# Kernel optimization log

Measured on AMD Instinct MI355X. Metric: run time of the kernel, lower is better.

The kernel has to match this reference:

```python
import jax, jax.numpy as jnp
import numpy as np

N = 100000
E = 1600000
F_IN = 16
HEADS = 4
OUT_CH = 32  # conv_filters[i] // heads = 128 // 4
HID = HEADS * OUT_CH  # 128
N_GRAPHS = 64
N_TARGETS = 4
EPS_BN = 1e-5


def setup_inputs() -> dict:
    key = jax.random.key(0)
    ks = jax.random.split(key, 32)
    glorot = lambda k, shp: jax.random.normal(k, shp, jnp.float32) * np.sqrt(2.0 / (shp[0] + shp[-1]))
    inp = {
        "node_features": jax.random.normal(ks[0], (N, F_IN), jnp.float32),
        "edge_index": jax.random.randint(ks[1], (2, E), 0, N, jnp.int64),
        "batch": jnp.sort(jax.random.randint(ks[2], (N,), 0, N_GRAPHS, jnp.int64)),
        # GAT layer 1: F_IN -> HEADS*OUT_CH
        "W1": glorot(ks[3], (F_IN, HID)),
        "b1": jnp.zeros((HID,), jnp.float32),
        "att_src1": glorot(ks[4], (HEADS, OUT_CH)),
        "att_dst1": glorot(ks[5], (HEADS, OUT_CH)),
        "bn_g1": jnp.ones((HID,), jnp.float32),
        "bn_b1": jnp.zeros((HID,), jnp.float32),
        # GAT layer 2: HID -> HID
        "W2": glorot(ks[6], (HID, HID)),
        "b2": jnp.zeros((HID,), jnp.float32),
        "att_src2": glorot(ks[7], (HEADS, OUT_CH)),
        "att_dst2": glorot(ks[8], (HEADS, OUT_CH)),
        "bn_g2": jnp.ones((HID,), jnp.float32),
        "bn_b2": jnp.zeros((HID,), jnp.float32),
        # dense head 128 -> 64 -> 32 -> 4
        "d1_W": glorot(ks[9], (HID, HID // 2)),
        "d1_b": jnp.zeros((HID // 2,), jnp.float32),
        "bn_g_d1": jnp.ones((HID // 2,), jnp.float32),
        "bn_b_d1": jnp.zeros((HID // 2,), jnp.float32),
        "d2_W": glorot(ks[10], (HID // 2, HID // 4)),
        "d2_b": jnp.zeros((HID // 4,), jnp.float32),
        "bn_g_d2": jnp.ones((HID // 4,), jnp.float32),
        "bn_b_d2": jnp.zeros((HID // 4,), jnp.float32),
        "fc_W": glorot(ks[11], (HID // 4, N_TARGETS)),
        "fc_b": jnp.zeros((N_TARGETS,), jnp.float32),
    }
    return inp


def batch_norm(x, gamma, beta):
    # training-mode BatchNorm1d: biased batch stats over dim 0
    mu = jnp.mean(x, axis=0)
    var = jnp.mean(jnp.square(x - mu), axis=0)
    return gamma * (x - mu) * jax.lax.rsqrt(var + EPS_BN) + beta


def gat_conv(x, src, dst, W, b, att_src, att_dst):
    # PyG GATConv (shared lin, concat heads): h = x @ W -> [N, H, C]
    h = (x @ W).reshape(-1, HEADS, OUT_CH)
    a_s = jnp.sum(h * att_src, axis=-1)  # [N, H]
    a_d = jnp.sum(h * att_dst, axis=-1)  # [N, H]
    e = jax.nn.leaky_relu(a_s[src] + a_d[dst], 0.2)  # [E, H]
    # softmax over incoming edges per destination node
    m = jax.ops.segment_max(e, dst, num_segments=N)
    m = jnp.where(jnp.isfinite(m), m, 0.0)
    w = jnp.exp(e - m[dst])
    s = jax.ops.segment_sum(w, dst, num_segments=N)
    alpha = w / (s[dst] + 1e-16)  # [E, H]
    out = jax.ops.segment_sum(h[src] * alpha[:, :, None], dst, num_segments=N)
    return out.reshape(-1, HID) + b


def reference(node_features, edge_index, batch,
              W1, b1, att_src1, att_dst1, bn_g1, bn_b1,
              W2, b2, att_src2, att_dst2, bn_g2, bn_b2,
              d1_W, d1_b, bn_g_d1, bn_b_d1,
              d2_W, d2_b, bn_g_d2, bn_b_d2,
              fc_W, fc_b):
    src, dst = edge_index[0], edge_index[1]
    x = gat_conv(node_features, src, dst, W1, b1, att_src1, att_dst1)
    x = jax.nn.relu(batch_norm(x, bn_g1, bn_b1))
    x = gat_conv(x, src, dst, W2, b2, att_src2, att_dst2)
    x = jax.nn.relu(batch_norm(x, bn_g2, bn_b2))
    # global mean pool over graphs
    sums = jax.ops.segment_sum(x, batch, num_segments=N_GRAPHS)
    cnt = jax.ops.segment_sum(jnp.ones((x.shape[0],), x.dtype), batch, num_segments=N_GRAPHS)
    g = sums / jnp.maximum(cnt, 1.0)[:, None]  # [G, HID]
    g = jax.nn.relu(batch_norm(g @ d1_W + d1_b, bn_g_d1, bn_b_d1))
    g = jax.nn.relu(batch_norm(g @ d2_W + d2_b, bn_g_d2, bn_b_d2))
    return g @ fc_W + fc_b
```

## Files before the change

### kernel.cpp

```cpp
#include <hip/hip_runtime.h>

#define HID 128
#define NG 64

__device__ __forceinline__ float lrelu(float v) { return v > 0.0f ? v : 0.2f * v; }

__device__ __forceinline__ unsigned int bf16rne(float f) {
    unsigned int u = __float_as_uint(f);
    return (u + 0x7fffu + ((u >> 16) & 1u)) >> 16;
}
__device__ __forceinline__ unsigned int packbf(float a, float b) {
    return bf16rne(a) | (bf16rne(b) << 16);
}

template <int K, bool BN>
__global__ __launch_bounds__(256) void k_gemm(const float* __restrict__ xin,
        const float* __restrict__ W,
        const double* __restrict__ bnsum, const float* __restrict__ gamma, const float* __restrict__ beta,
        const float* __restrict__ attS, const float* __restrict__ attD,
        unsigned short* __restrict__ h, float* __restrict__ as_, float* __restrict__ ad_, int N)
{
    __shared__ float xs[64][K];
    __shared__ __align__(16) float sc_s[K];
    __shared__ __align__(16) float sh_s[K];
    constexpr int K4 = K / 4;
    int t = threadIdx.x;
    int cq = t & 31;
    int nr = t >> 5;

    if (BN) {
        if (t < K) {
            double mu = bnsum[t] / (double)N;
            double var = bnsum[K + t] / (double)N - mu * mu;
            if (var < 0.0) var = 0.0;
            double rs = 1.0 / sqrt(var + 1e-5);
            float sc = (float)((double)gamma[t] * rs);
            sc_s[t] = sc;
            sh_s[t] = beta[t] - (float)mu * sc;
        }
        __syncthreads();
    }

    float4 atS = ((const float4*)attS)[cq];
    float4 atD = ((const float4*)attD)[cq];

    for (int n0 = blockIdx.x * 64; n0 < N; n0 += gridDim.x * 64) {
        int nrem = N - n0; if (nrem > 64) nrem = 64;
        for (int idx = t; idx < 64 * K4; idx += 256) {
            int n = idx / K4, k4 = idx % K4;
            float4 v = make_float4(0.f, 0.f, 0.f, 0.f);
            if (n < nrem) {
                v = ((const float4*)(xin + (size_t)(n0 + n) * K))[k4];
                if (BN) {
                    float4 sc = ((const float4*)sc_s)[k4];
                    float4 sh = ((const float4*)sh_s)[k4];
                    v.x = fmaf(v.x, sc.x, sh.x); v.x = v.x > 0.f ? v.x : 0.f;
                    v.y = fmaf(v.y, sc.y, sh.y); v.y = v.y > 0.f ? v.y : 0.f;
                    v.z = fmaf(v.z, sc.z, sh.z); v.z = v.z > 0.f ? v.z : 0.f;
                    v.w = fmaf(v.w, sc.w, sh.w); v.w = v.w > 0.f ? v.w : 0.f;
                }
            }
            *(float4*)(&xs[n][k4 * 4]) = v;
        }
        __syncthreads();

        float4 acc[8];
#pragma unroll
        for (int j = 0; j < 8; ++j) acc[j] = make_float4(0.f, 0.f, 0.f, 0.f);

        const float4* W4 = (const float4*)W;
#pragma unroll 2
        for (int k4 = 0; k4 < K4; ++k4) {
            float4 w0 = W4[(k4 * 4 + 0) * 32 + cq];
            float4 w1 = W4[(k4 * 4 + 1) * 32 + cq];
            float4 w2 = W4[(k4 * 4 + 2) * 32 + cq];
            float4 w3 = W4[(k4 * 4 + 3) * 32 + cq];
#pragma unroll
            for (int j = 0; j < 8; ++j) {
                float4 xv = *(const float4*)(&xs[nr * 8 + j][k4 * 4]);
                acc[j].x = fmaf(xv.x, w0.x, acc[j].x);
                acc[j].y = fmaf(xv.x, w0.y, acc[j].y);
                acc[j].z = fmaf(xv.x, w0.z, acc[j].z);
                acc[j].w = fmaf(xv.x, w0.w, acc[j].w);
                acc[j].x = fmaf(xv.y, w1.x, acc[j].x);
                acc[j].y = fmaf(xv.y, w1.y, acc[j].y);
                acc[j].z = fmaf(xv.y, w1.z, acc[j].z);
                acc[j].w = fmaf(xv.y, w1.w, acc[j].w);
                acc[j].x = fmaf(xv.z, w2.x, acc[j].x);
                acc[j].y = fmaf(xv.z, w2.y, acc[j].y);
                acc[j].z = fmaf(xv.z, w2.z, acc[j].z);
                acc[j].w = fmaf(xv.z, w2.w, acc[j].w);
                acc[j].x = fmaf(xv.w, w3.x, acc[j].x);
                acc[j].y = fmaf(xv.w, w3.y, acc[j].y);
                acc[j].z = fmaf(xv.w, w3.z, acc[j].z);
                acc[j].w = fmaf(xv.w, w3.w, acc[j].w);
            }
        }

#pragma unroll
        for (int j = 0; j < 8; ++j) {
            int n = nr * 8 + j;
            bool ok = (n < nrem);
            if (ok) {
                unsigned int lo = packbf(acc[j].x, acc[j].y);
                unsigned int hi = packbf(acc[j].z, acc[j].w);
                ((uint2*)(h + (size_t)(n0 + n) * 128))[cq] = make_uint2(lo, hi);
            }
            float ps = acc[j].x * atS.x + acc[j].y * atS.y + acc[j].z * atS.z + acc[j].w * atS.w;
            float pd = acc[j].x * atD.x + acc[j].y * atD.y + acc[j].z * atD.z + acc[j].w * atD.w;
            ps += __shfl_xor(ps, 1); pd += __shfl_xor(pd, 1);
            ps += __shfl_xor(ps, 2); pd += __shfl_xor(pd, 2);
            ps += __shfl_xor(ps, 4); pd += __shfl_xor(pd, 4);
            if (ok && (cq & 7) == 0) {
                int hd = cq >> 3;
                as_[(size_t)(n0 + n) * 4 + hd] = ps;
                ad_[(size_t)(n0 + n) * 4 + hd] = pd;
            }
        }
        __syncthreads();
    }
}

__global__ __launch_bounds__(256) void k_bhist(const int* __restrict__ ei,
        int* __restrict__ bSize, int E, int nB)
{
    __shared__ int hist[1024];
    int t = threadIdx.x;
    for (int i = t; i < nB; i += 256) hist[i] = 0;
    __syncthreads();
    int chunk = (E + gridDim.x - 1) / gridDim.x;
    int lo = blockIdx.x * chunk, hi = lo + chunk; if (hi > E) hi = E;
    for (int e = lo + t; e < hi; e += 256) atomicAdd(&hist[ei[E + e] >> 8], 1);
    __syncthreads();
    for (int i = t; i < nB; i += 256) { int c = hist[i]; if (c) atomicAdd(&bSize[i], c); }
}

__global__ __launch_bounds__(512) void k_bscan(const int* __restrict__ bSize,
        int* __restrict__ bOff, int* __restrict__ bCur, int nB)
{
    __shared__ int part[512];
    int t = threadIdx.x;
    part[t] = (t < nB) ? bSize[t] : 0;
    __syncthreads();
    for (int off = 1; off < 512; off <<= 1) {
        int u = (t >= off) ? part[t - off] : 0;
        __syncthreads();
        part[t] += u;
        __syncthreads();
    }
    int ex = (t == 0) ? 0 : part[t - 1];
    if (t < nB) { bOff[t] = ex; bCur[t] = ex; }
    if (t == nB - 1) bOff[nB] = part[t];
}

__global__ __launch_bounds__(256) void k_part(const int* __restrict__ ei,
        int* __restrict__ bCur, unsigned int* __restrict__ bucketBuf, int E, int nB)
{
    __shared__ int hist[1024];
    __shared__ int base[1024];
    int t = threadIdx.x;
    int chunk = (E + gridDim.x - 1) / gridDim.x;
    int lo = blockIdx.x * chunk, hi = lo + chunk; if (hi > E) hi = E;
    for (int i = t; i < nB; i += 256) hist[i] = 0;
    __syncthreads();
    for (int e = lo + t; e < hi; e += 256) atomicAdd(&hist[ei[E + e] >> 8], 1);
    __syncthreads();
    for (int i = t; i < nB; i += 256) {
        int c = hist[i];
        base[i] = c ? atomicAdd(&bCur[i], c) : 0;
        hist[i] = 0;
    }
    __syncthreads();
    for (int e = lo + t; e < hi; e += 256) {
        int s = ei[e], d = ei[E + e];
        int b = d >> 8;
        int pos = base[b] + atomicAdd(&hist[b], 1);
        bucketBuf[pos] = ((unsigned)(d & 255) << 24) | (unsigned)s;
    }
}

__global__ __launch_bounds__(256) void k_build(const unsigned int* __restrict__ bucketBuf,
        const int* __restrict__ bOff, int* __restrict__ rowPtr, int* __restrict__ sSrc, int N)
{
    __shared__ int lhist[256];
    __shared__ int sOut[8192];
    int b = blockIdx.x;
    int dlo = b << 8;
    int dhi = dlo + 256; if (dhi > N) dhi = N;
    int base = bOff[b], end = bOff[b + 1];
    int sz = end - base;
    int t = threadIdx.x;
    lhist[t] = 0;
    __syncthreads();
    for (int i = t; i < sz; i += 256) {
        atomicAdd(&lhist[bucketBuf[base + i] >> 24], 1);
    }
    __syncthreads();
    for (int off = 1; off < 256; off <<= 1) {
        int u = (t >= off) ? lhist[t - off] : 0;
        __syncthreads();
        lhist[t] += u;
        __syncthreads();
    }
    int pfx = (t == 0) ? 0 : lhist[t - 1];
    if (dlo + t < dhi) rowPtr[dlo + t] = base + pfx;
    if (t == 0 && dhi == N) rowPtr[N] = end;
    __syncthreads();
    lhist[t] = pfx;
    __syncthreads();
    if (sz <= 8192) {
        for (int i = t; i < sz; i += 256) {
            unsigned int p = bucketBuf[base + i];
            int pos = atomicAdd(&lhist[p >> 24], 1);
            sOut[pos] = (int)(p & 0xffffffu);
        }
        __syncthreads();
        for (int i = t; i < sz; i += 256) sSrc[base + i] = sOut[i];
    } else {
        for (int i = t; i < sz; i += 256) {
            unsigned int p = bucketBuf[base + i];
            int pos = atomicAdd(&lhist[p >> 24], 1);
            sSrc[base + pos] = (int)(p & 0xffffffu);
        }
    }
}

__global__ __launch_bounds__(256) void k_agg(const int* __restrict__ rowPtr,
        const int* __restrict__ sSrc,
        const float* __restrict__ as_, const float* __restrict__ ad_,
        const unsigned short* __restrict__ h, float* __restrict__ out, int N)
{
    __shared__ float wst[8][64][4];
    int t = threadIdx.x;
    int lane = t & 31;
    int g = t >> 5;
    int d = blockIdx.x * 8 + g;
    bool valid = (d < N);
    int b0 = 0, deg = 0;
    float4 adv = make_float4(0.f, 0.f, 0.f, 0.f);
    if (valid) { b0 = rowPtr[d]; deg = rowPtr[d + 1] - b0; adv = ((const float4*)ad_)[d]; }

    float4 sm = make_float4(0.f, 0.f, 0.f, 0.f);
    for (int e = lane; e < deg; e += 32) {
        int s = sSrc[b0 + e];
        float4 a = ((const float4*)as_)[s];
        float4 w;
        w.x = __expf(lrelu(a.x + adv.x));
        w.y = __expf(lrelu(a.y + adv.y));
        w.z = __expf(lrelu(a.z + adv.z));
        w.w = __expf(lrelu(a.w + adv.w));
        if (e < 64) *(float4*)(&wst[g][e][0]) = w;
        sm.x += w.x; sm.y += w.y; sm.z += w.z; sm.w += w.w;
    }
#pragma unroll
    for (int off = 1; off < 32; off <<= 1) {
        sm.x += __shfl_xor(sm.x, off);
        sm.y += __shfl_xor(sm.y, off);
        sm.z += __shfl_xor(sm.z, off);
        sm.w += __shfl_xor(sm.w, off);
    }
    __syncthreads();

    int hd = lane >> 3;
    float sumh = (hd == 0) ? sm.x : (hd == 1) ? sm.y : (hd == 2) ? sm.z : sm.w;
    float advh = (hd == 0) ? adv.x : (hd == 1) ? adv.y : (hd == 2) ? adv.z : adv.w;
    float inv = 1.f / (sumh + 1e-16f);

    const uint2* h2 = (const uint2*)h;
    const int* sp = sSrc + b0;
    float4 acc = make_float4(0.f, 0.f, 0.f, 0.f);
    int dc = deg < 64 ? deg : 64;
    int j = 0;
#define AGG1(S, W) { uint2 u = h2[(size_t)(S) * 32 + lane]; \
        acc.x = fmaf((W), __uint_as_float(u.x << 16), acc.x); \
        acc.y = fmaf((W), __uint_as_float(u.x & 0xffff0000u), acc.y); \
        acc.z = fmaf((W), __uint_as_float(u.y << 16), acc.z); \
        acc.w = fmaf((W), __uint_as_float(u.y & 0xffff0000u), acc.w); }
    for (; j + 8 <= dc; j += 8) {
        int s0 = sp[j], s1 = sp[j+1], s2 = sp[j+2], s3 = sp[j+3];
        int s4 = sp[j+4], s5 = sp[j+5], s6 = sp[j+6], s7 = sp[j+7];
        float w0 = wst[g][j][hd],   w1 = wst[g][j+1][hd], w2 = wst[g][j+2][hd], w3 = wst[g][j+3][hd];
        float w4 = wst[g][j+4][hd], w5 = wst[g][j+5][hd], w6 = wst[g][j+6][hd], w7 = wst[g][j+7][hd];
        uint2 u0 = h2[(size_t)s0*32+lane], u1 = h2[(size_t)s1*32+lane];
        uint2 u2 = h2[(size_t)s2*32+lane], u3 = h2[(size_t)s3*32+lane];
        uint2 u4 = h2[(size_t)s4*32+lane], u5 = h2[(size_t)s5*32+lane];
        uint2 u6 = h2[(size_t)s6*32+lane], u7 = h2[(size_t)s7*32+lane];
        acc.x = fmaf(w0, __uint_as_float(u0.x << 16), acc.x);
        acc.y = fmaf(w0, __uint_as_float(u0.x & 0xffff0000u), acc.y);
        acc.z = fmaf(w0, __uint_as_float(u0.y << 16), acc.z);
        acc.w = fmaf(w0, __uint_as_float(u0.y & 0xffff0000u), acc.w);
        acc.x = fmaf(w1, __uint_as_float(u1.x << 16), acc.x);
        acc.y = fmaf(w1, __uint_as_float(u1.x & 0xffff0000u), acc.y);
        acc.z = fmaf(w1, __uint_as_float(u1.y << 16), acc.z);
        acc.w = fmaf(w1, __uint_as_float(u1.y & 0xffff0000u), acc.w);
        acc.x = fmaf(w2, __uint_as_float(u2.x << 16), acc.x);
        acc.y = fmaf(w2, __uint_as_float(u2.x & 0xffff0000u), acc.y);
        acc.z = fmaf(w2, __uint_as_float(u2.y << 16), acc.z);
        acc.w = fmaf(w2, __uint_as_float(u2.y & 0xffff0000u), acc.w);
        acc.x = fmaf(w3, __uint_as_float(u3.x << 16), acc.x);
        acc.y = fmaf(w3, __uint_as_float(u3.x & 0xffff0000u), acc.y);
        acc.z = fmaf(w3, __uint_as_float(u3.y << 16), acc.z);
        acc.w = fmaf(w3, __uint_as_float(u3.y & 0xffff0000u), acc.w);
        acc.x = fmaf(w4, __uint_as_float(u4.x << 16), acc.x);
        acc.y = fmaf(w4, __uint_as_float(u4.x & 0xffff0000u), acc.y);
        acc.z = fmaf(w4, __uint_as_float(u4.y << 16), acc.z);
        acc.w = fmaf(w4, __uint_as_float(u4.y & 0xffff0000u), acc.w);
        acc.x = fmaf(w5, __uint_as_float(u5.x << 16), acc.x);
        acc.y = fmaf(w5, __uint_as_float(u5.x & 0xffff0000u), acc.y);
        acc.z = fmaf(w5, __uint_as_float(u5.y << 16), acc.z);
        acc.w = fmaf(w5, __uint_as_float(u5.y & 0xffff0000u), acc.w);
        acc.x = fmaf(w6, __uint_as_float(u6.x << 16), acc.x);
        acc.y = fmaf(w6, __uint_as_float(u6.x & 0xffff0000u), acc.y);
        acc.z = fmaf(w6, __uint_as_float(u6.y << 16), acc.z);
        acc.w = fmaf(w6, __uint_as_float(u6.y & 0xffff0000u), acc.w);
        acc.x = fmaf(w7, __uint_as_float(u7.x << 16), acc.x);
        acc.y = fmaf(w7, __uint_as_float(u7.x & 0xffff0000u), acc.y);
        acc.z = fmaf(w7, __uint_as_float(u7.y << 16), acc.z);
        acc.w = fmaf(w7, __uint_as_float(u7.y & 0xffff0000u), acc.w);
    }
    for (; j < dc; ++j) {
        float w = wst[g][j][hd];
        AGG1(sp[j], w);
    }
    for (; j < deg; ++j) {
        int s = sp[j];
        float w = __expf(lrelu(as_[(size_t)s * 4 + hd] + advh));
        AGG1(s, w);
    }
#undef AGG1
    if (valid) {
        acc.x *= inv; acc.y *= inv; acc.z *= inv; acc.w *= inv;
        ((float4*)out)[(size_t)d * 32 + lane] = acc;
    }
}

__global__ __launch_bounds__(256) void k_bnstats(const float* __restrict__ x,
        double* __restrict__ sums, int N)
{
    __shared__ float4 r1[256], r2[256];
    int t = threadIdx.x;
    int lane = t & 31;
    int rg = t >> 5;
    const float4* x4 = (const float4*)x;
    float4 s1 = make_float4(0.f, 0.f, 0.f, 0.f);
    float4 s2 = make_float4(0.f, 0.f, 0.f, 0.f);
    for (int n = blockIdx.x * 8 + rg; n < N; n += gridDim.x * 8) {
        float4 v = x4[(size_t)n * 32 + lane];
        s1.x += v.x; s1.y += v.y; s1.z += v.z; s1.w += v.w;
        s2.x += v.x * v.x; s2.y += v.y * v.y; s2.z += v.z * v.z; s2.w += v.w * v.w;
    }
    r1[t] = s1; r2[t] = s2;
    __syncthreads();
    if (t < 32) {
        float4 a = r1[t], b = r2[t];
        for (int k = 1; k < 8; ++k) {
            float4 c = r1[t + 32 * k], e = r2[t + 32 * k];
            a.x += c.x; a.y += c.y; a.z += c.z; a.w += c.w;
            b.x += e.x; b.y += e.y; b.z += e.z; b.w += e.w;
        }
        atomicAdd(&sums[t * 4 + 0], (double)a.x);
        atomicAdd(&sums[t * 4 + 1], (double)a.y);
        atomicAdd(&sums[t * 4 + 2], (double)a.z);
        atomicAdd(&sums[t * 4 + 3], (double)a.w);
        atomicAdd(&sums[128 + t * 4 + 0], (double)b.x);
        atomicAdd(&sums[128 + t * 4 + 1], (double)b.y);
        atomicAdd(&sums[128 + t * 4 + 2], (double)b.z);
        atomicAdd(&sums[128 + t * 4 + 3], (double)b.w);
    }
}

__global__ __launch_bounds__(128) void k_pool(const float* __restrict__ x,
        const int* __restrict__ batch,
        const double* __restrict__ bnsum, const float* __restrict__ gamma, const float* __restrict__ beta,
        float* __restrict__ gsum, float* __restrict__ gcnt, int N)
{
    __shared__ __align__(16) float sc_s[128];
    __shared__ __align__(16) float sh_s[128];
    int t = threadIdx.x;
    {
        double mu = bnsum[t] / (double)N;
        double var = bnsum[128 + t] / (double)N - mu * mu;
        if (var < 0.0) var = 0.0;
        double rs = 1.0 / sqrt(var + 1e-5);
        float sc = (float)((double)gamma[t] * rs);
        sc_s[t] = sc;
        sh_s[t] = beta[t] - (float)mu * sc;
    }
    __syncthreads();

    int lane = t & 31;
    int r = t >> 5;
    int n0 = blockIdx.x * 64;
    if (n0 >= N) return;
    int n1 = n0 + 64; if (n1 > N) n1 = N;
    float4 sc = ((const float4*)sc_s)[lane];
    float4 sh = ((const float4*)sh_s)[lane];
    float4 acc = make_float4(0.f, 0.f, 0.f, 0.f);
    int cnt = 0, cur = -1;
    for (int n = n0 + r; n < n1; n += 4) {
        int g = batch[n];
        if (g != cur) {
            if (cur >= 0) {
                atomicAdd(&gsum[cur * 128 + lane * 4 + 0], acc.x);
                atomicAdd(&gsum[cur * 128 + lane * 4 + 1], acc.y);
                atomicAdd(&gsum[cur * 128 + lane * 4 + 2], acc.z);
                atomicAdd(&gsum[cur * 128 + lane * 4 + 3], acc.w);
                if (lane == 0) atomicAdd(&gcnt[cur], (float)cnt);
            }
            acc = make_float4(0.f, 0.f, 0.f, 0.f); cnt = 0; cur = g;
        }
        float4 v = ((const float4*)x)[(size_t)n * 32 + lane];
        v.x = fmaf(v.x, sc.x, sh.x); v.x = v.x > 0.f ? v.x : 0.f;
        v.y = fmaf(v.y, sc.y, sh.y); v.y = v.y > 0.f ? v.y : 0.f;
        v.z = fmaf(v.z, sc.z, sh.z); v.z = v.z > 0.f ? v.z : 0.f;
        v.w = fmaf(v.w, sc.w, sh.w); v.w = v.w > 0.f ? v.w : 0.f;
        acc.x += v.x; acc.y += v.y; acc.z += v.z; acc.w += v.w;
        cnt++;
    }
    if (cur >= 0) {
        atomicAdd(&gsum[cur * 128 + lane * 4 + 0], acc.x);
        atomicAdd(&gsum[cur * 128 + lane * 4 + 1], acc.y);
        atomicAdd(&gsum[cur * 128 + lane * 4 + 2], acc.z);
        atomicAdd(&gsum[cur * 128 + lane * 4 + 3], acc.w);
        if (lane == 0) atomicAdd(&gcnt[cur], (float)cnt);
    }
}

__global__ __launch_bounds__(256) void k_head(const float* __restrict__ gsum, const float* __restrict__ gcnt,
        const float* __restrict__ d1W, const float* __restrict__ d1b,
        const float* __restrict__ g_d1, const float* __restrict__ b_d1,
        const float* __restrict__ d2W, const float* __restrict__ d2b,
        const float* __restrict__ g_d2, const float* __restrict__ b_d2,
        const float* __restrict__ fcW, const float* __restrict__ fcb,
        float* __restrict__ out)
{
    __shared__ float G[64 * 128];
    __shared__ float Y1[64 * 64];
    __shared__ float Y2[64 * 32];
    int t = threadIdx.x;
    for (int i = t; i < 64 * 128; i += 256) {
        int g = i >> 7;
        float cv = gcnt[g]; if (cv < 1.f) cv = 1.f;
        G[i] = gsum[i] / cv;
    }
    __syncthreads();
    for (int i = t; i < 64 * 64; i += 256) {
        int r = i >> 6, j = i & 63;
        float a = 0.f;
        for (int k = 0; k < 128; ++k) a = fmaf(G[r * 128 + k], d1W[k * 64 + j], a);
        Y1[i] = a + d1b[j];
    }
    __syncthreads();
    if (t < 64) {
        float s1 = 0.f, s2 = 0.f;
        for (int r = 0; r < 64; ++r) { float v = Y1[r * 64 + t]; s1 += v; s2 += v * v; }
        float mu = s1 / 64.f, var = s2 / 64.f - mu * mu; if (var < 0.f) var = 0.f;
        float rs = 1.0f / sqrtf(var + 1e-5f);
        float scv = g_d1[t] * rs, shv = b_d1[t] - mu * scv;
        for (int r = 0; r < 64; ++r) {
            float v = fmaf(Y1[r * 64 + t], scv, shv);
            Y1[r * 64 + t] = v > 0.f ? v : 0.f;
        }
    }
    __syncthreads();
    for (int i = t; i < 64 * 32; i += 256) {
        int r = i >> 5, j = i & 31;
        float a = 0.f;
        for (int k = 0; k < 64; ++k) a = fmaf(Y1[r * 64 + k], d2W[k * 32 + j], a);
        Y2[i] = a + d2b[j];
    }
    __syncthreads();
    if (t < 32) {
        float s1 = 0.f, s2 = 0.f;
        for (int r = 0; r < 64; ++r) { float v = Y2[r * 32 + t]; s1 += v; s2 += v * v; }
        float mu = s1 / 64.f, var = s2 / 64.f - mu * mu; if (var < 0.f) var = 0.f;
        float rs = 1.0f / sqrtf(var + 1e-5f);
        float scv = g_d2[t] * rs, shv = b_d2[t] - mu * scv;
        for (int r = 0; r < 64; ++r) {
            float v = fmaf(Y2[r * 32 + t], scv, shv);
            Y2[r * 32 + t] = v > 0.f ? v : 0.f;
        }
    }
    __syncthreads();
    {
        int r = t >> 2, j = t & 3;
        float a = 0.f;
        for (int k = 0; k < 32; ++k) a = fmaf(Y2[r * 32 + k], fcW[k * 4 + j], a);
        out[t] = a + fcb[j];
    }
}

extern "C" void kernel_launch(void* const* d_in, const int* in_sizes, int n_in,
                              void* d_out, int out_size, void* d_ws, size_t ws_size,
                              hipStream_t stream) {
    const int N = in_sizes[0] / 16;
    const int E = in_sizes[1] / 2;
    const int nB = (N + 255) >> 8;

    const float* x        = (const float*)d_in[0];
    const int*   ei       = (const int*)d_in[1];
    const int*   batch    = (const int*)d_in[2];
    const float* W1       = (const float*)d_in[3];
    const float* att_s1   = (const float*)d_in[5];
    const float* att_d1   = (const float*)d_in[6];
    const float* bn_g1    = (const float*)d_in[7];
    const float* bn_b1    = (const float*)d_in[8];
    const float* W2       = (const float*)d_in[9];
    const float* att_s2   = (const float*)d_in[11];
    const float* att_d2   = (const float*)d_in[12];
    const float* bn_g2    = (const float*)d_in[13];
    const float* bn_b2    = (const float*)d_in[14];
    const float* d1W      = (const float*)d_in[15];
    const float* d1b      = (const float*)d_in[16];
    const float* g_d1     = (const float*)d_in[17];
    const float* b_d1     = (const float*)d_in[18];
    const float* d2W      = (const float*)d_in[19];
    const float* d2b      = (const float*)d_in[20];
    const float* g_d2     = (const float*)d_in[21];
    const float* b_d2     = (const float*)d_in[22];
    const float* fcW      = (const float*)d_in[23];
    const float* fcb      = (const float*)d_in[24];
    float* out = (float*)d_out;

    float* ws = (float*)d_ws;
    size_t o = 0;
    unsigned short* hbuf = (unsigned short*)(ws + o); o += (size_t)N * 64;
    float* outb   = ws + o;  o += (size_t)N * 128;
    float* as_    = ws + o;  o += (size_t)N * 4;
    float* ad_    = ws + o;  o += (size_t)N * 4;
    size_t zoff = o;
    double* bnsumA = (double*)(ws + o); o += 512;
    double* bnsumB = (double*)(ws + o); o += 512;
    float* gsum   = ws + o;  o += 64 * 128;
    float* gcnt   = ws + o;  o += 64;
    int*   bSize  = (int*)(ws + o); o += 1024;
    size_t zbytes = (o - zoff) * 4;
    int* rowPtr   = (int*)(ws + o); o += (size_t)N + 1;
    int* sSrc     = (int*)(ws + o); o += E;
    int* bOff     = (int*)(ws + o); o += 1025;
    int* bCur     = (int*)(ws + o); o += 1024;
    unsigned int* bucketBuf = (unsigned int*)(ws + o); o += E;

    hipMemsetAsync(ws + zoff, 0, zbytes, stream);

    k_bhist<<<256, 256, 0, stream>>>(ei, bSize, E, nB);
    k_bscan<<<1, 512, 0, stream>>>(bSize, bOff, bCur, nB);
    k_part<<<256, 256, 0, stream>>>(ei, bCur, bucketBuf, E, nB);
    k_build<<<nB, 256, 0, stream>>>(bucketBuf, bOff, rowPtr, sSrc, N);

    int gemm_grid = (N + 63) / 64;
    int agg_grid = (N + 7) / 8;

    k_gemm<16, false><<<gemm_grid, 256, 0, stream>>>(x, W1, nullptr, nullptr, nullptr,
            att_s1, att_d1, hbuf, as_, ad_, N);
    k_agg<<<agg_grid, 256, 0, stream>>>(rowPtr, sSrc, as_, ad_, hbuf, outb, N);
    k_bnstats<<<512, 256, 0, stream>>>(outb, bnsumA, N);

    k_gemm<128, true><<<gemm_grid, 256, 0, stream>>>(outb, W2, bnsumA, bn_g1, bn_b1,
            att_s2, att_d2, hbuf, as_, ad_, N);
    k_agg<<<agg_grid, 256, 0, stream>>>(rowPtr, sSrc, as_, ad_, hbuf, outb, N);
    k_bnstats<<<512, 256, 0, stream>>>(outb, bnsumB, N);

    k_pool<<<(N + 63) / 64, 128, 0, stream>>>(outb, batch, bnsumB, bn_g2, bn_b2, gsum, gcnt, N);
    k_head<<<1, 256, 0, stream>>>(gsum, gcnt, d1W, d1b, g_d1, b_d1,
                                  d2W, d2b, g_d2, b_d2, fcW, fcb, out);
}
```

Measured before the change: 605.8 us.

## Use 16 lanes per node with 16-byte gathers and recompute attention weights

The aggregation kernel now assigns 16 lanes per destination node instead of 32, so each lane loads a uint4 (8 bf16 values) per neighbor and keeps two float4 accumulators. The shared-memory cache of edge weights and the block-wide barrier are removed. Weights are recomputed per head in the gather loop from as_, which adds an extra scalar load and exp per edge. The aim is to halve the wavefronts per node, widen memory transactions and drop the synchronisation, at the cost of redundant exp work and a shorter unroll of 4.

```diff
diff --git a/kernel.cpp b/kernel.cpp
--- a/kernel.cpp
+++ b/kernel.cpp
@@ -230,108 +230,100 @@
         const float* __restrict__ as_, const float* __restrict__ ad_,
         const unsigned short* __restrict__ h, float* __restrict__ out, int N)
 {
-    __shared__ float wst[8][64][4];
-    int t = threadIdx.x;
-    int lane = t & 31;
-    int g = t >> 5;
-    int d = blockIdx.x * 8 + g;
-    bool valid = (d < N);
-    int b0 = 0, deg = 0;
-    float4 adv = make_float4(0.f, 0.f, 0.f, 0.f);
-    if (valid) { b0 = rowPtr[d]; deg = rowPtr[d + 1] - b0; adv = ((const float4*)ad_)[d]; }
+    int t = threadIdx.x;
+    int l = t & 15;
+    int d = blockIdx.x * 16 + (t >> 4);
+    if (d >= N) return;
+    int hd = l >> 2;
+    int b0 = rowPtr[d], b1 = rowPtr[d + 1];
+    float4 adv = ((const float4*)ad_)[d];
 
     float4 sm = make_float4(0.f, 0.f, 0.f, 0.f);
-    for (int e = lane; e < deg; e += 32) {
-        int s = sSrc[b0 + e];
+    for (int j = b0 + l; j < b1; j += 16) {
+        int s = sSrc[j];
         float4 a = ((const float4*)as_)[s];
-        float4 w;
-        w.x = __expf(lrelu(a.x + adv.x));
-        w.y = __expf(lrelu(a.y + adv.y));
-        w.z = __expf(lrelu(a.z + adv.z));
-        w.w = __expf(lrelu(a.w + adv.w));
-        if (e < 64) *(float4*)(&wst[g][e][0]) = w;
-        sm.x += w.x; sm.y += w.y; sm.z += w.z; sm.w += w.w;
+        sm.x += __expf(lrelu(a.x + adv.x));
+        sm.y += __expf(lrelu(a.y + adv.y));
+        sm.z += __expf(lrelu(a.z + adv.z));
+        sm.w += __expf(lrelu(a.w + adv.w));
     }
 #pragma unroll
-    for (int off = 1; off < 32; off <<= 1) {
+    for (int off = 1; off < 16; off <<= 1) {
         sm.x += __shfl_xor(sm.x, off);
         sm.y += __shfl_xor(sm.y, off);
         sm.z += __shfl_xor(sm.z, off);
         sm.w += __shfl_xor(sm.w, off);
     }
-    __syncthreads();
-
-    int hd = lane >> 3;
     float sumh = (hd == 0) ? sm.x : (hd == 1) ? sm.y : (hd == 2) ? sm.z : sm.w;
     float advh = (hd == 0) ? adv.x : (hd == 1) ? adv.y : (hd == 2) ? adv.z : adv.w;
     float inv = 1.f / (sumh + 1e-16f);
 
-    const uint2* h2 = (const uint2*)h;
-    const int* sp = sSrc + b0;
-    float4 acc = make_float4(0.f, 0.f, 0.f, 0.f);
-    int dc = deg < 64 ? deg : 64;
-    int j = 0;
-#define AGG1(S, W) { uint2 u = h2[(size_t)(S) * 32 + lane]; \
-        acc.x = fmaf((W), __uint_as_float(u.x << 16), acc.x); \
-        acc.y = fmaf((W), __uint_as_float(u.x & 0xffff0000u), acc.y); \
-        acc.z = fmaf((W), __uint_as_float(u.y << 16), acc.z); \
-        acc.w = fmaf((W), __uint_as_float(u.y & 0xffff0000u), acc.w); }
-    for (; j + 8 <= dc; j += 8) {
-        int s0 = sp[j], s1 = sp[j+1], s2 = sp[j+2], s3 = sp[j+3];
-        int s4 = sp[j+4], s5 = sp[j+5], s6 = sp[j+6], s7 = sp[j+7];
-        float w0 = wst[g][j][hd],   w1 = wst[g][j+1][hd], w2 = wst[g][j+2][hd], w3 = wst[g][j+3][hd];
-        float w4 = wst[g][j+4][hd], w5 = wst[g][j+5][hd], w6 = wst[g][j+6][hd], w7 = wst[g][j+7][hd];
-        uint2 u0 = h2[(size_t)s0*32+lane], u1 = h2[(size_t)s1*32+lane];
-        uint2 u2 = h2[(size_t)s2*32+lane], u3 = h2[(size_t)s3*32+lane];
-        uint2 u4 = h2[(size_t)s4*32+lane], u5 = h2[(size_t)s5*32+lane];
-        uint2 u6 = h2[(size_t)s6*32+lane], u7 = h2[(size_t)s7*32+lane];
-        acc.x = fmaf(w0, __uint_as_float(u0.x << 16), acc.x);
-        acc.y = fmaf(w0, __uint_as_float(u0.x & 0xffff0000u), acc.y);
-        acc.z = fmaf(w0, __uint_as_float(u0.y << 16), acc.z);
-        acc.w = fmaf(w0, __uint_as_float(u0.y & 0xffff0000u), acc.w);
-        acc.x = fmaf(w1, __uint_as_float(u1.x << 16), acc.x);
-        acc.y = fmaf(w1, __uint_as_float(u1.x & 0xffff0000u), acc.y);
-        acc.z = fmaf(w1, __uint_as_float(u1.y << 16), acc.z);
-        acc.w = fmaf(w1, __uint_as_float(u1.y & 0xffff0000u), acc.w);
-        acc.x = fmaf(w2, __uint_as_float(u2.x << 16), acc.x);
-        acc.y = fmaf(w2, __uint_as_float(u2.x & 0xffff0000u), acc.y);
-        acc.z = fmaf(w2, __uint_as_float(u2.y << 16), acc.z);
-        acc.w = fmaf(w2, __uint_as_float(u2.y & 0xffff0000u), acc.w);
-        acc.x = fmaf(w3, __uint_as_float(u3.x << 16), acc.x);
-        acc.y = fmaf(w3, __uint_as_float(u3.x & 0xffff0000u), acc.y);
-        acc.z = fmaf(w3, __uint_as_float(u3.y << 16), acc.z);
-        acc.w = fmaf(w3, __uint_as_float(u3.y & 0xffff0000u), acc.w);
-        acc.x = fmaf(w4, __uint_as_float(u4.x << 16), acc.x);
-        acc.y = fmaf(w4, __uint_as_float(u4.x & 0xffff0000u), acc.y);
-        acc.z = fmaf(w4, __uint_as_float(u4.y << 16), acc.z);
-        acc.w = fmaf(w4, __uint_as_float(u4.y & 0xffff0000u), acc.w);
-        acc.x = fmaf(w5, __uint_as_float(u5.x << 16), acc.x);
-        acc.y = fmaf(w5, __uint_as_float(u5.x & 0xffff0000u), acc.y);
-        acc.z = fmaf(w5, __uint_as_float(u5.y << 16), acc.z);
-        acc.w = fmaf(w5, __uint_as_float(u5.y & 0xffff0000u), acc.w);
-        acc.x = fmaf(w6, __uint_as_float(u6.x << 16), acc.x);
-        acc.y = fmaf(w6, __uint_as_float(u6.x & 0xffff0000u), acc.y);
-        acc.z = fmaf(w6, __uint_as_float(u6.y << 16), acc.z);
-        acc.w = fmaf(w6, __uint_as_float(u6.y & 0xffff0000u), acc.w);
-        acc.x = fmaf(w7, __uint_as_float(u7.x << 16), acc.x);
-        acc.y = fmaf(w7, __uint_as_float(u7.x & 0xffff0000u), acc.y);
-        acc.z = fmaf(w7, __uint_as_float(u7.y << 16), acc.z);
-        acc.w = fmaf(w7, __uint_as_float(u7.y & 0xffff0000u), acc.w);
-    }
-    for (; j < dc; ++j) {
-        float w = wst[g][j][hd];
-        AGG1(sp[j], w);
-    }
-    for (; j < deg; ++j) {
-        int s = sp[j];
+    const uint4* h4 = (const uint4*)h;
+    float4 acc0 = make_float4(0.f, 0.f, 0.f, 0.f);
+    float4 acc1 = make_float4(0.f, 0.f, 0.f, 0.f);
+#define AGG1(S, W) { uint4 u = h4[(size_t)(S) * 16 + l]; \
+        acc0.x = fmaf((W), __uint_as_float(u.x << 16), acc0.x); \
+        acc0.y = fmaf((W), __uint_as_float(u.x & 0xffff0000u), acc0.y); \
+        acc0.z = fmaf((W), __uint_as_float(u.y << 16), acc0.z); \
+        acc0.w = fmaf((W), __uint_as_float(u.y & 0xffff0000u), acc0.w); \
+        acc1.x = fmaf((W), __uint_as_float(u.z << 16), acc1.x); \
+        acc1.y = fmaf((W), __uint_as_float(u.z & 0xffff0000u), acc1.y); \
+        acc1.z = fmaf((W), __uint_as_float(u.w << 16), acc1.z); \
+        acc1.w = fmaf((W), __uint_as_float(u.w & 0xffff0000u), acc1.w); }
+    int j = b0;
+    for (; j + 4 <= b1; j += 4) {
+        int s0 = sSrc[j], s1 = sSrc[j + 1], s2 = sSrc[j + 2], s3 = sSrc[j + 3];
+        float w0 = __expf(lrelu(as_[(size_t)s0 * 4 + hd] + advh));
+        float w1 = __expf(lrelu(as_[(size_t)s1 * 4 + hd] + advh));
+        float w2 = __expf(lrelu(as_[(size_t)s2 * 4 + hd] + advh));
+        float w3 = __expf(lrelu(as_[(size_t)s3 * 4 + hd] + advh));
+        uint4 u0 = h4[(size_t)s0 * 16 + l];
+        uint4 u1 = h4[(size_t)s1 * 16 + l];
+        uint4 u2 = h4[(size_t)s2 * 16 + l];
+        uint4 u3 = h4[(size_t)s3 * 16 + l];
+        acc0.x = fmaf(w0, __uint_as_float(u0.x << 16), acc0.x);
+        acc0.y = fmaf(w0, __uint_as_float(u0.x & 0xffff0000u), acc0.y);
+        acc0.z = fmaf(w0, __uint_as_float(u0.y << 16), acc0.z);
+        acc0.w = fmaf(w0, __uint_as_float(u0.y & 0xffff0000u), acc0.w);
+        acc1.x = fmaf(w0, __uint_as_float(u0.z << 16), acc1.x);
+        acc1.y = fmaf(w0, __uint_as_float(u0.z & 0xffff0000u), acc1.y);
+        acc1.z = fmaf(w0, __uint_as_float(u0.w << 16), acc1.z);
+        acc1.w = fmaf(w0, __uint_as_float(u0.w & 0xffff0000u), acc1.w);
+        acc0.x = fmaf(w1, __uint_as_float(u1.x << 16), acc0.x);
+        acc0.y = fmaf(w1, __uint_as_float(u1.x & 0xffff0000u), acc0.y);
+        acc0.z = fmaf(w1, __uint_as_float(u1.y << 16), acc0.z);
+        acc0.w = fmaf(w1, __uint_as_float(u1.y & 0xffff0000u), acc0.w);
+        acc1.x = fmaf(w1, __uint_as_float(u1.z << 16), acc1.x);
+        acc1.y = fmaf(w1, __uint_as_float(u1.z & 0xffff0000u), acc1.y);
+        acc1.z = fmaf(w1, __uint_as_float(u1.w << 16), acc1.z);
+        acc1.w = fmaf(w1, __uint_as_float(u1.w & 0xffff0000u), acc1.w);
+        acc0.x = fmaf(w2, __uint_as_float(u2.x << 16), acc0.x);
+        acc0.y = fmaf(w2, __uint_as_float(u2.x & 0xffff0000u), acc0.y);
+        acc0.z = fmaf(w2, __uint_as_float(u2.y << 16), acc0.z);
+        acc0.w = fmaf(w2, __uint_as_float(u2.y & 0xffff0000u), acc0.w);
+        acc1.x = fmaf(w2, __uint_as_float(u2.z << 16), acc1.x);
+        acc1.y = fmaf(w2, __uint_as_float(u2.z & 0xffff0000u), acc1.y);
+        acc1.z = fmaf(w2, __uint_as_float(u2.w << 16), acc1.z);
+        acc1.w = fmaf(w2, __uint_as_float(u2.w & 0xffff0000u), acc1.w);
+        acc0.x = fmaf(w3, __uint_as_float(u3.x << 16), acc0.x);
+        acc0.y = fmaf(w3, __uint_as_float(u3.x & 0xffff0000u), acc0.y);
+        acc0.z = fmaf(w3, __uint_as_float(u3.y << 16), acc0.z);
+        acc0.w = fmaf(w3, __uint_as_float(u3.y & 0xffff0000u), acc0.w);
+        acc1.x = fmaf(w3, __uint_as_float(u3.z << 16), acc1.x);
+        acc1.y = fmaf(w3, __uint_as_float(u3.z & 0xffff0000u), acc1.y);
+        acc1.z = fmaf(w3, __uint_as_float(u3.w << 16), acc1.z);
+        acc1.w = fmaf(w3, __uint_as_float(u3.w & 0xffff0000u), acc1.w);
+    }
+    for (; j < b1; ++j) {
+        int s = sSrc[j];
         float w = __expf(lrelu(as_[(size_t)s * 4 + hd] + advh));
         AGG1(s, w);
     }
 #undef AGG1
-    if (valid) {
-        acc.x *= inv; acc.y *= inv; acc.z *= inv; acc.w *= inv;
-        ((float4*)out)[(size_t)d * 32 + lane] = acc;
-    }
+    acc0.x *= inv; acc0.y *= inv; acc0.z *= inv; acc0.w *= inv;
+    acc1.x *= inv; acc1.y *= inv; acc1.z *= inv; acc1.w *= inv;
+    ((float4*)out)[(size_t)d * 32 + l * 2] = acc0;
+    ((float4*)out)[(size_t)d * 32 + l * 2 + 1] = acc1;
 }
 
 __global__ __launch_bounds__(256) void k_bnstats(const float* __restrict__ x,
@@ -549,7 +541,7 @@
     k_build<<<nB, 256, 0, stream>>>(bucketBuf, bOff, rowPtr, sSrc, N);
 
     int gemm_grid = (N + 63) / 64;
-    int agg_grid = (N + 7) / 8;
+    int agg_grid = (N + 15) / 16;
 
     k_gemm<16, false><<<gemm_grid, 256, 0, stream>>>(x, W1, nullptr, nullptr, nullptr,
             att_s1, att_d1, hbuf, as_, ad_, N);
```

Result: faster. 574.1 us (-5.2%).
